# Performance work log

Measured on AMD Instinct MI355X. Metric: run time of the kernel, lower is better.

The kernel has to match this reference:

```python
import jax, jax.numpy as jnp
import numpy as np

N_QUBITS = 18
BATCH = 64
NUM_LAYERS = 4


def setup_inputs() -> dict:
    key = jax.random.key(0)
    k1, k2 = jax.random.split(key)
    inputs = jax.random.normal(k1, (BATCH, N_QUBITS), dtype=jnp.float32)
    params = jax.random.normal(k2, (NUM_LAYERS, N_QUBITS, 1), dtype=jnp.float32)
    return {"inputs": inputs, "params": params}


def _apply_shared_1q(state, U, q, B):
    # state: (B, 2^n) complex; U: (2,2) complex; qubit q (wire 0 = most significant)
    st = state.reshape(B, 2 ** q, 2, -1)
    return jnp.einsum('ij,bxjy->bxiy', U, st).reshape(B, -1)


def _apply_batched_1q(state, U, q, B):
    # U: (B,2,2) complex, per-sample gate
    st = state.reshape(B, 2 ** q, 2, -1)
    return jnp.einsum('bij,bxjy->bxiy', U, st).reshape(B, -1)


def _apply_cnot(state, q, B):
    # control = q, target = q+1: flip target amplitudes where control == 1
    st = state.reshape(B, 2 ** q, 2, 2, -1)
    flipped = jnp.flip(st[:, :, 1], axis=2)  # (B, 2^q, 2, rest)
    st = jnp.concatenate([st[:, :, :1], flipped[:, :, None]], axis=2)
    return st.reshape(B, -1)


def reference(inputs, params):
    B, n = inputs.shape
    L = params.shape[0]
    state = jnp.zeros((B, 2 ** n), dtype=jnp.complex64).at[:, 0].set(1.0)

    # data-encoding RX(inputs[:, q]) on each qubit (per-sample angles)
    half = (inputs * 0.5).astype(jnp.float32)
    c = jnp.cos(half).astype(jnp.complex64)          # (B, n)
    s = (-1j * jnp.sin(half)).astype(jnp.complex64)  # (B, n)
    for q in range(n):
        U = jnp.stack([jnp.stack([c[:, q], s[:, q]], axis=-1),
                       jnp.stack([s[:, q], c[:, q]], axis=-1)], axis=-2)  # (B,2,2)
        state = _apply_batched_1q(state, U, q, B)

    # variational blocks: RY per qubit (shared angle) + CNOT ladder
    for layer in range(L):
        for q in range(n):
            th = params[layer, q, 0] * 0.5
            cc = jnp.cos(th).astype(jnp.complex64)
            ss = jnp.sin(th).astype(jnp.complex64)
            U = jnp.stack([jnp.stack([cc, -ss]), jnp.stack([ss, cc])])  # (2,2)
            state = _apply_shared_1q(state, U, q, B)
        for q in range(n - 1):
            state = _apply_cnot(state, q, B)
    return state
```

## Files before the change

### kernel.cpp

```cpp
#include <hip/hip_runtime.h>
#include <utility>

#define NQ 18
#define BATCH 64

#define VT_OFFC (1u << 24)
#define CS_OFFC (VT_OFFC + BATCH * NQ * 4)

typedef float v2f __attribute__((ext_vector_type(2)));

__device__ __forceinline__ float2 cmulf(float2 a, float2 b) {
    return make_float2(a.x * b.x - a.y * b.y, a.x * b.y + a.y * b.x);
}

template<class F, int... Is>
__device__ __forceinline__ void unroll_impl(F f, std::integer_sequence<int, Is...>) {
    (f(std::integral_constant<int, Is>{}), ...);
}
template<int N, class F>
__device__ __forceinline__ void unroll(F f) {
    unroll_impl(f, std::make_integer_sequence<int, N>{});
}

struct Gate { int k, p; };
constexpr Gate GT[54] = {
    {2,13},{2,14},{2,15},{2,16},{2,17}, {3,14},{3,15},{3,16},{3,17}, {4,15},{4,16},{4,17},
    {2,11},{2,12}, {3,12},{3,13}, {4,13},{4,14},
    {2,8},{2,9},{2,10}, {3,9},{3,10},{3,11}, {4,10},{4,11},{4,12},
    {2,5},{2,6},{2,7}, {3,6},{3,7},{3,8}, {4,7},{4,8},{4,9},
    {2,0},{2,1},{2,2},{2,3},{2,4},
    {3,0},{3,1},{3,2},{3,3},{3,4},{3,5},
    {4,0},{4,1},{4,2},{4,3},{4,4},{4,5},{4,6},
};
constexpr unsigned gmask(Gate g) {
    return g.k == 2 ? (g.p >= 1 ? 3u << (g.p - 1) : 1u)
         : g.k == 3 ? (g.p >= 2 ? 5u << (g.p - 2) : 1u << g.p)
         : (g.p >= 3 ? 15u << (g.p - 3) : (1u << (g.p + 1)) - 1u);
}
constexpr unsigned gorient(Gate g) {
    return g.k == 2 ? (0x3FFFFu & ~((1u << g.p) - 1u))
         : g.k == 3 ? ((0x15555u << g.p) & 0x3FFFFu)
         : ((0x33333u << g.p) & 0x3FFFFu);
}
constexpr int gcsi(Gate g) { return (g.k - 2) * NQ + (17 - g.p); }

constexpr bool clsPresent(int OFF, int NG, int k, int r) {
    for (int i = 0; i < NG; ++i) {
        Gate g = GT[OFF + i];
        if (g.k == k) {
            int rr = (k == 2) ? 0 : (k == 3) ? (g.p & 1) : (g.p & 3);
            if (rr == r) return true;
        }
    }
    return false;
}

template<int WL, int OFF, int NG, int NR>
__device__ __forceinline__ void apply_gates2(v2f* A, unsigned xfix, const float* csn) {
    constexpr int NR2 = NR / 2;
    constexpr unsigned HIM = 0x3FFFFu & ~((((unsigned)NR) << WL) - 1u);

    int par2 = 0, par3[2] = {0, 0}, par4[4] = {0, 0, 0, 0};
    if constexpr (clsPresent(OFF, NG, 2, 0)) par2    = __popc(xfix & HIM) & 1;
    if constexpr (clsPresent(OFF, NG, 3, 0)) par3[0] = __popc(xfix & (HIM & 0x15555u)) & 1;
    if constexpr (clsPresent(OFF, NG, 3, 1)) par3[1] = __popc(xfix & (HIM & 0x2AAAAu)) & 1;
    if constexpr (clsPresent(OFF, NG, 4, 0)) par4[0] = __popc(xfix & (HIM & 0x33333u)) & 1;
    if constexpr (clsPresent(OFF, NG, 4, 1)) par4[1] = __popc(xfix & (HIM & 0x66666u)) & 1;
    if constexpr (clsPresent(OFF, NG, 4, 2)) par4[2] = __popc(xfix & (HIM & 0xCCCCCu)) & 1;
    if constexpr (clsPresent(OFF, NG, 4, 3)) par4[3] = __popc(xfix & (HIM & 0x99999u)) & 1;

    unroll<NG>([&](auto I) {
        constexpr Gate g = GT[OFF + I.value];
        constexpr unsigned m   = gmask(g);
        constexpr unsigned O   = gorient(g);
        constexpr unsigned mr  = (m >> WL) & (unsigned)(NR - 1);
        constexpr unsigned hb  = 1u << (g.p - WL);
        constexpr unsigned Or  = (O >> WL) & (unsigned)(NR - 1);
        constexpr unsigned Orf = Or >> 1;
        constexpr bool     Or0 = (Or & 1u) != 0;
        constexpr int clsR = (g.k == 2) ? 0 : (g.k == 3) ? (g.p & 1) : (g.p & 3);
        float c = csn[2 * gcsi(g)], s = csn[2 * gcsi(g) + 1];
        int par = (g.k == 2) ? par2 : (g.k == 3) ? par3[clsR] : par4[clsR];
        float psv = par ? -s : s;
        float msv = -psv;
        v2f cv; cv.x = c; cv.y = c;
        if constexpr ((mr & 1u) == 0u) {
            constexpr unsigned hbf = hb >> 1, mrf = mr >> 1;
            unroll<NR2>([&](auto RR) {
                constexpr int R = RR.value;
                if constexpr ((R & (int)hbf) == 0) {
                    constexpr int R2 = R ^ (int)mrf;
                    constexpr bool fl0 = (__builtin_popcount((unsigned)R & Orf) & 1) != 0;
                    constexpr bool fl1 = fl0 != Or0;
                    v2f sev; sev.x = fl0 ? msv : psv; sev.y = fl1 ? msv : psv;
                    v2f x0 = A[R], x1 = A[R2];
                    A[R]  = cv * x0 - sev * x1;
                    A[R2] = sev * x0 + cv * x1;
                }
            });
        } else if constexpr (mr == 1u) {
            unroll<NR2>([&](auto RR) {
                constexpr int R = RR.value;
                constexpr bool fl0 = (__builtin_popcount((unsigned)R & Orf) & 1) != 0;
                float se0 = fl0 ? msv : psv;
                v2f v = A[R], nv;
                nv.x = c * v.x - se0 * v.y;
                nv.y = se0 * v.x + c * v.y;
                A[R] = nv;
            });
        } else {
            constexpr unsigned hbf = hb >> 1, mrf = mr >> 1;
            unroll<NR2>([&](auto RR) {
                constexpr int R = RR.value;
                if constexpr ((R & (int)hbf) == 0) {
                    constexpr int R2 = R ^ (int)mrf;
                    constexpr bool fl0 = (__builtin_popcount((unsigned)R & Orf) & 1) != 0;
                    constexpr bool fl1 = fl0 != Or0;
                    v2f sev; sev.x = fl0 ? msv : psv; sev.y = fl1 ? msv : psv;
                    v2f x0 = A[R], x1 = A[R2];
                    v2f x1s = __builtin_shufflevector(x1, x1, 1, 0);
                    v2f t   = sev * x0;
                    v2f ts  = __builtin_shufflevector(t, t, 1, 0);
                    A[R]  = cv * x0 - sev * x1s;
                    A[R2] = ts + cv * x1;
                }
            });
        }
    });
}

template<int J>
__device__ __forceinline__ float geta(const v2f* A) {
    if constexpr (J & 1) return A[J >> 1].y; else return A[J >> 1].x;
}
template<int J>
__device__ __forceinline__ void seta(v2f* A, float v) {
    if constexpr (J & 1) A[J >> 1].y = v; else A[J >> 1].x = v;
}

__device__ __forceinline__ float4 perm4(float4 r, int k) {
    float t0 = r.x, t1 = r.y, t2 = r.z, t3 = r.w;
    if (k & 1) { float x; x=t0;t0=t1;t1=x; x=t2;t2=t3;t3=x; }
    if (k & 2) { float x; x=t0;t0=t2;t2=x; x=t1;t1=t3;t3=x; }
    return make_float4(t0, t1, t2, t3);
}

__global__ void k_prep(const float* __restrict__ inputs, const float* __restrict__ params,
                       float* __restrict__ ws) {
    int t = blockIdx.x * blockDim.x + threadIdx.x;
    if (t < BATCH * NQ) {
        int q = t % NQ;
        float x = 0.5f * inputs[t];
        float cx = cosf(x), sx = sinf(x);
        float th = 0.5f * params[q];
        float c = cosf(th), s = sinf(th);
        float* v = ws + VT_OFFC + t * 4;
        v[0] = c * cx;  v[1] = s * sx;
        v[2] = s * cx;  v[3] = -c * sx;
    } else if (t < BATCH * NQ + 54) {
        int i = t - BATCH * NQ;
        float th = 0.5f * params[NQ + i];
        ws[CS_OFFC + 2 * i]     = cosf(th);
        ws[CS_OFFC + 2 * i + 1] = sinf(th);
    }
}

__global__ __launch_bounds__(256) void k_passA(const float* __restrict__ ws_tab,
                                               float* __restrict__ ws) {
    __shared__ __align__(16) float lds[16384];
    const int b  = blockIdx.x >> 4;
    const int c4 = blockIdx.x & 15;
    const int t  = threadIdx.x;
    const float* vt  = ws_tab + VT_OFFC + b * NQ * 4;
    const float* csn = ws_tab + CS_OFFC;

    unsigned xf0 = (unsigned)c4 | ((unsigned)t << 4);
    float2 f[12];
    #pragma unroll
    for (int i = 0; i < 12; ++i) {
        int bit = (xf0 >> i) & 1;
        const float* vq = vt + (17 - i) * 4 + bit * 2;
        f[i] = make_float2(vq[0], vq[1]);
    }
    f[0] = cmulf(f[0], f[1]);  f[2] = cmulf(f[2], f[3]);
    f[4] = cmulf(f[4], f[5]);  f[6] = cmulf(f[6], f[7]);
    f[8] = cmulf(f[8], f[9]);  f[10] = cmulf(f[10], f[11]);
    f[0] = cmulf(f[0], f[2]);  f[4] = cmulf(f[4], f[6]);  f[8] = cmulf(f[8], f[10]);
    f[0] = cmulf(f[0], f[4]);
    float2 pf = cmulf(f[0], f[8]);

    float2 ca[32];
    ca[0] = pf;
    #pragma unroll
    for (int bp = 0; bp < 5; ++bp) {
        const float* vq = vt + (5 - bp) * 4;
        float2 v0 = make_float2(vq[0], vq[1]), v1 = make_float2(vq[2], vq[3]);
        #pragma unroll
        for (int i = (1 << bp) - 1; i >= 0; --i) {
            float2 base = ca[i];
            ca[i + (1 << bp)] = cmulf(base, v1);
            ca[i] = cmulf(base, v0);
        }
    }
    v2f A[32];
    {
        const float* vq = vt;
        float2 v0 = make_float2(vq[0], vq[1]), v1 = make_float2(vq[2], vq[3]);
        unroll<16>([&](auto RR) {
            constexpr int R = RR.value;
            A[R].x      = ca[2*R].x   * v0.x - ca[2*R].y   * v0.y;
            A[R].y      = ca[2*R+1].x * v0.x - ca[2*R+1].y * v0.y;
            A[16+R].x   = ca[2*R].x   * v1.x - ca[2*R].y   * v1.y;
            A[16+R].y   = ca[2*R+1].x * v1.x - ca[2*R+1].y * v1.y;
        });
    }
    apply_gates2<12, 0, 12, 64>(A, xf0, csn);

    unsigned St = (unsigned)t ^ ((unsigned)t >> 6);
    unroll<8>([&](auto Rr) {
        constexpr int r = Rr.value;
        unsigned br = St ^ (unsigned)((r << 8) | (r << 2));
        unroll<8>([&](auto Qq) {
            constexpr int q = Qq.value;
            lds[br + (q << 11)] = geta<q * 8 + r>(A);
        });
    });
    __syncthreads();

    unsigned Sb1 = (unsigned)(t & 63) | ((unsigned)(t >> 6) << 12);
    unroll<64>([&](auto J) {
        constexpr unsigned K = (unsigned)((J.value << 6) | (J.value & 31));
        seta<J.value>(A, lds[Sb1 ^ K]);
    });
    unsigned xf1 = (unsigned)c4 | ((unsigned)(t & 63) << 4) | ((unsigned)(t >> 6) << 16);
    apply_gates2<10, 12, 6, 64>(A, xf1, csn);
    unroll<64>([&](auto J) {
        constexpr unsigned K = (unsigned)((J.value << 6) | (J.value & 31));
        lds[Sb1 ^ K] = geta<J.value>(A);
    });
    __syncthreads();

    unsigned Sb2 = ((unsigned)(t & 7) | ((unsigned)(t >> 3) << 9))
                 ^ ((((unsigned)t >> 3) & 3u) << 3);
    unroll<64>([&](auto J) {
        constexpr unsigned K = (unsigned)((J.value << 3) | (J.value >> 3));
        seta<J.value>(A, lds[Sb2 ^ K]);
    });
    unsigned xf2 = (unsigned)c4 | ((unsigned)(t & 7) << 4) | ((unsigned)(t >> 3) << 13);
    apply_gates2<7, 18, 9, 64>(A, xf2, csn);
    unroll<64>([&](auto J) {
        constexpr unsigned K = (unsigned)((J.value << 3) | (J.value >> 3));
        lds[Sb2 ^ K] = geta<J.value>(A);
    });
    __syncthreads();

    unsigned Sb3 = ((unsigned)t << 6) ^ ((unsigned)t & 31u);
    unroll<64>([&](auto J) {
        seta<J.value>(A, lds[Sb3 ^ (unsigned)J.value]);
    });
    unsigned xf3 = (unsigned)c4 | ((unsigned)t << 10);
    apply_gates2<4, 27, 9, 64>(A, xf3, csn);

    float* wp = ws + (((size_t)b << 18) | ((size_t)(t >> 6) << 16)
                      | ((size_t)c4 << 9) | (size_t)(t & 63));
    unroll<64>([&](auto J) {
        constexpr int j = J.value;
        constexpr unsigned off = (unsigned)(((j >> 3) << 6) | ((j & 7) << 13));
        wp[off] = geta<j>(A);
    });
}

__global__ __launch_bounds__(256) void k_passB(const float* __restrict__ ws,
                                               float* __restrict__ out) {
    __shared__ __align__(16) float lds[8192];
    const int t = threadIdx.x;
    const int b = blockIdx.x >> 3;
    const int m = ((blockIdx.x & 7) << 8) | t;
    const float* csn = ws + CS_OFFC;
    unsigned Mv = (unsigned)m ^ ((unsigned)m >> 4);

    const float* rb = ws + (((size_t)b << 18)
                    | (size_t)((Mv >> 3) & 7u)
                    | ((size_t)((Mv >> 6) & 7u) << 3)
                    | ((size_t)(Mv & 7u) << 6)
                    | ((size_t)((Mv >> 9) & 3u) << 16));
    v2f A[64];
    unroll<128>([&](auto N) {
        constexpr int n = N.value;
        constexpr unsigned off = (unsigned)(((n & 15) << 9) | ((n >> 4) << 13));
        seta<n>(A, rb[off]);
    });
    apply_gates2<0, 36, 18, 128>(A, Mv << 7, csn);

    unsigned cc = ((unsigned)m & 15u) << 3;
    float* obb = out + (((size_t)b << NQ) | ((size_t)(blockIdx.x & 7) << 15));
    const unsigned w6 = (unsigned)(t & 63);
    const unsigned Sw = (w6 << 7) ^ ((w6 << 1) & 28u);
    const int myQ = t >> 6;
    #pragma unroll
    for (int Q = 0; Q < 4; ++Q) {
        if (myQ == Q) {
            unroll<32>([&](auto Qd) {
                constexpr int n0 = Qd.value << 2;
                unsigned nx = (unsigned)n0 ^ cc;
                unsigned D  = (nx ^ (nx >> 4)) & 127u;
                unsigned Bq = Sw ^ (D & ~3u);
                float4 v = make_float4(geta<n0>(A), geta<n0 ^ 1>(A),
                                       geta<n0 ^ 2>(A), geta<n0 ^ 3>(A));
                *(float4*)&lds[Bq] = perm4(v, (int)(D & 3u));
            });
        }
        __syncthreads();
        float* ohQ = obb + ((size_t)Q << 13);
        unroll<8>([&](auto I) {
            constexpr int i = I.value;
            unsigned p0 = ((unsigned)(i * 256) + (unsigned)t) << 2;
            unsigned z0 = p0 ^ ((p0 >> 6) & 28u);
            *(float4*)&ohQ[z0] = *(const float4*)&lds[p0];
        });
        __syncthreads();
    }
}

__global__ __launch_bounds__(256) void k_init_f(const float* __restrict__ inputs,
                                                const float* __restrict__ params,
                                                float* __restrict__ S) {
    __shared__ float2 vt[2][NQ];
    int g = blockIdx.x * 256 + threadIdx.x;
    int b = g >> 13;
    int t = threadIdx.x;
    if (t < NQ) {
        float x = 0.5f * inputs[b * NQ + t];
        float cx = cosf(x), sx = sinf(x);
        float th = 0.5f * params[t];
        float c = cosf(th), s = sinf(th);
        vt[0][t] = make_float2(c * cx,  s * sx);
        vt[1][t] = make_float2(s * cx, -c * sx);
    }
    __syncthreads();
    unsigned OW = (unsigned)(g & 0x1FFF);
    unsigned iu = OW ^ (OW >> 1);
    int pu = OW & 1;
    float2 p = make_float2(1.f, 0.f);
    #pragma unroll
    for (int q = 0; q <= 12; ++q) {
        int bit = (iu >> (12 - q)) & 1;
        p = cmulf(p, vt[bit][q]);
    }
    float2 a[32];
    a[0] = p;
    #pragma unroll
    for (int bp = 0; bp < 5; ++bp) {
        float2 v0 = vt[0][17 - bp], v1 = vt[1][17 - bp];
        if (bp == 4 && pu) { float2 tt = v0; v0 = v1; v1 = tt; }
        #pragma unroll
        for (int i = (1 << bp) - 1; i >= 0; --i) {
            float2 base = a[i];
            a[i + (1 << bp)] = cmulf(base, v1);
            a[i] = cmulf(base, v0);
        }
    }
    float* outp = S + ((size_t)b << NQ) + ((size_t)OW << 5);
    #pragma unroll
    for (int oj = 0; oj < 32; oj += 4) {
        int k0 = oj ^ (oj >> 1);
        *(float4*)(outp + oj) = make_float4(a[k0].x, a[k0 ^ 1].x, a[k0 ^ 3].x, a[k0 ^ 2].x);
    }
}

template<int P>
__global__ __launch_bounds__(256) void k_pass_f(const float* __restrict__ params,
                                                float* __restrict__ S, int layer) {
    int g = blockIdx.x * 256 + threadIdx.x;
    float cg[6], sg[6];
    #pragma unroll
    for (int i = 0; i < 6; ++i) {
        float th = 0.5f * params[layer * NQ + 6 * P + i];
        cg[i] = cosf(th); sg[i] = sinf(th);
    }
    size_t base; int hm;
    constexpr int STR = (P == 0) ? 4096 : (P == 1) ? 64 : 1;
    if constexpr (P == 0) {
        base = ((size_t)(g >> 12) << NQ) | (size_t)(g & 0xFFF);
        hm = 0;
    } else if constexpr (P == 1) {
        base = ((size_t)(g >> 12) << NQ) | ((size_t)((g >> 6) & 63) << 12) | (size_t)(g & 63);
        hm = (g >> 6) & 1;
    } else {
        base = (size_t)g << 6;
        hm = g & 1;
    }
    float a[64];
    if constexpr (P == 2) {
        #pragma unroll
        for (int j = 0; j < 64; j += 4) {
            float4 w = *(const float4*)(S + base + j);
            a[j] = w.x; a[j + 1] = w.y; a[j + 2] = w.z; a[j + 3] = w.w;
        }
    } else {
        #pragma unroll
        for (int j = 0; j < 64; ++j) a[j] = S[base + (size_t)j * STR];
    }
    #pragma unroll
    for (int i = 0; i < 6; ++i) {
        int mm = 32 >> i;
        #pragma unroll
        for (int r = 0; r < 64; ++r) if (!(r & mm)) {
            float x0 = a[r], x1 = a[r | mm];
            a[r]      = cg[i] * x0 - sg[i] * x1;
            a[r | mm] = sg[i] * x0 + cg[i] * x1;
        }
    }
    if (hm) {
        #pragma unroll
        for (int r = 0; r < 32; ++r) { float tt = a[r]; a[r] = a[r ^ 32]; a[r ^ 32] = tt; }
    }
    if constexpr (P == 2) {
        #pragma unroll
        for (int oj = 0; oj < 64; oj += 4) {
            int k0 = oj ^ (oj >> 1);
            *(float4*)(S + base + oj) = make_float4(a[k0], a[k0 ^ 1], a[k0 ^ 3], a[k0 ^ 2]);
        }
    } else {
        #pragma unroll
        for (int oj = 0; oj < 64; ++oj)
            S[base + (size_t)oj * STR] = a[oj ^ (oj >> 1)];
    }
}

extern "C" void kernel_launch(void* const* d_in, const int* in_sizes, int n_in,
                              void* d_out, int out_size, void* d_ws, size_t ws_size,
                              hipStream_t stream) {
    const float* inputs = (const float*)d_in[0];
    const float* params = (const float*)d_in[1];
    float* out = (float*)d_out;
    float* ws  = (float*)d_ws;
    const size_t need = (size_t)4 * ((1ull << 24) + BATCH * NQ * 4 + 108);

    if (ws_size >= need) {
        k_prep<<<5, 256, 0, stream>>>(inputs, params, ws);
        k_passA<<<BATCH * 16, 256, 0, stream>>>(ws, ws);
        k_passB<<<512, 256, 0, stream>>>(ws, out);
    } else {
        k_init_f<<<2048, 256, 0, stream>>>(inputs, params, out);
        for (int layer = 1; layer < 4; ++layer) {
            k_pass_f<0><<<1024, 256, 0, stream>>>(params, out, layer);
            k_pass_f<1><<<1024, 256, 0, stream>>>(params, out, layer);
            k_pass_f<2><<<1024, 256, 0, stream>>>(params, out, layer);
        }
    }
}
```

Measured before the change: 76.66 us.

## Restructure passA to 512 threads with 32 amplitudes per thread and more LDS stages

Pass A now runs 512 threads per block, each holding 32 amplitudes instead of 64, and the gate schedule is re-split into six register-local stages with five LDS transposes instead of four stages with three. The global write layout of the intermediate state changes, and pass B's read addressing is updated to match. The aim is to cut register pressure and raise occupancy and latency hiding. The cost is more shared-memory round trips and barriers per block.

```diff
diff --git a/kernel.cpp b/kernel.cpp
--- a/kernel.cpp
+++ b/kernel.cpp
@@ -24,10 +24,12 @@
 
 struct Gate { int k, p; };
 constexpr Gate GT[54] = {
-    {2,13},{2,14},{2,15},{2,16},{2,17}, {3,14},{3,15},{3,16},{3,17}, {4,15},{4,16},{4,17},
-    {2,11},{2,12}, {3,12},{3,13}, {4,13},{4,14},
-    {2,8},{2,9},{2,10}, {3,9},{3,10},{3,11}, {4,10},{4,11},{4,12},
-    {2,5},{2,6},{2,7}, {3,6},{3,7},{3,8}, {4,7},{4,8},{4,9},
+    {2,14},{2,15},{2,16},{2,17}, {3,15},{3,16},{3,17}, {4,16},{4,17},
+    {2,12},{2,13}, {3,13},{3,14}, {4,14},{4,15},
+    {2,10},{2,11}, {3,11},{3,12}, {4,12},{4,13},
+    {2,8},{2,9}, {3,9},{3,10}, {4,10},{4,11},
+    {2,6},{2,7}, {3,7},{3,8}, {4,8},{4,9},
+    {2,5}, {3,6}, {4,7},
     {2,0},{2,1},{2,2},{2,3},{2,4},
     {3,0},{3,1},{3,2},{3,3},{3,4},{3,5},
     {4,0},{4,1},{4,2},{4,3},{4,4},{4,5},{4,6},
@@ -165,7 +167,7 @@
     }
 }
 
-__global__ __launch_bounds__(256) void k_passA(const float* __restrict__ ws_tab,
+__global__ __launch_bounds__(512) void k_passA(const float* __restrict__ ws_tab,
                                                float* __restrict__ ws) {
     __shared__ __align__(16) float lds[16384];
     const int b  = blockIdx.x >> 4;
@@ -175,25 +177,24 @@
     const float* csn = ws_tab + CS_OFFC;
 
     unsigned xf0 = (unsigned)c4 | ((unsigned)t << 4);
-    float2 f[12];
-    #pragma unroll
-    for (int i = 0; i < 12; ++i) {
+    float2 f[13];
+    #pragma unroll
+    for (int i = 0; i < 13; ++i) {
         int bit = (xf0 >> i) & 1;
         const float* vq = vt + (17 - i) * 4 + bit * 2;
         f[i] = make_float2(vq[0], vq[1]);
     }
-    f[0] = cmulf(f[0], f[1]);  f[2] = cmulf(f[2], f[3]);
-    f[4] = cmulf(f[4], f[5]);  f[6] = cmulf(f[6], f[7]);
-    f[8] = cmulf(f[8], f[9]);  f[10] = cmulf(f[10], f[11]);
-    f[0] = cmulf(f[0], f[2]);  f[4] = cmulf(f[4], f[6]);  f[8] = cmulf(f[8], f[10]);
-    f[0] = cmulf(f[0], f[4]);
+    f[0]=cmulf(f[0],f[1]); f[2]=cmulf(f[2],f[3]); f[4]=cmulf(f[4],f[5]);
+    f[6]=cmulf(f[6],f[7]); f[8]=cmulf(f[8],f[9]); f[10]=cmulf(f[10],f[11]);
+    f[0]=cmulf(f[0],f[2]); f[4]=cmulf(f[4],f[6]); f[8]=cmulf(f[8],f[10]);
+    f[0]=cmulf(f[0],f[4]); f[8]=cmulf(f[8],f[12]);
     float2 pf = cmulf(f[0], f[8]);
 
-    float2 ca[32];
+    float2 ca[16];
     ca[0] = pf;
     #pragma unroll
-    for (int bp = 0; bp < 5; ++bp) {
-        const float* vq = vt + (5 - bp) * 4;
+    for (int bp = 0; bp < 4; ++bp) {
+        const float* vq = vt + (3 - bp) * 4;
         float2 v0 = make_float2(vq[0], vq[1]), v1 = make_float2(vq[2], vq[3]);
         #pragma unroll
         for (int i = (1 << bp) - 1; i >= 0; --i) {
@@ -202,71 +203,87 @@
             ca[i] = cmulf(base, v0);
         }
     }
-    v2f A[32];
+    v2f A[16];
     {
-        const float* vq = vt;
+        const float* vq = vt + 4 * 4;
         float2 v0 = make_float2(vq[0], vq[1]), v1 = make_float2(vq[2], vq[3]);
         unroll<16>([&](auto RR) {
             constexpr int R = RR.value;
-            A[R].x      = ca[2*R].x   * v0.x - ca[2*R].y   * v0.y;
-            A[R].y      = ca[2*R+1].x * v0.x - ca[2*R+1].y * v0.y;
-            A[16+R].x   = ca[2*R].x   * v1.x - ca[2*R].y   * v1.y;
-            A[16+R].y   = ca[2*R+1].x * v1.x - ca[2*R+1].y * v1.y;
+            A[R].x = ca[R].x * v0.x - ca[R].y * v0.y;
+            A[R].y = ca[R].x * v1.x - ca[R].y * v1.y;
         });
     }
-    apply_gates2<12, 0, 12, 64>(A, xf0, csn);
-
-    unsigned St = (unsigned)t ^ ((unsigned)t >> 6);
-    unroll<8>([&](auto Rr) {
-        constexpr int r = Rr.value;
-        unsigned br = St ^ (unsigned)((r << 8) | (r << 2));
-        unroll<8>([&](auto Qq) {
-            constexpr int q = Qq.value;
-            lds[br + (q << 11)] = geta<q * 8 + r>(A);
-        });
-    });
-    __syncthreads();
-
-    unsigned Sb1 = (unsigned)(t & 63) | ((unsigned)(t >> 6) << 12);
-    unroll<64>([&](auto J) {
-        constexpr unsigned K = (unsigned)((J.value << 6) | (J.value & 31));
-        seta<J.value>(A, lds[Sb1 ^ K]);
-    });
-    unsigned xf1 = (unsigned)c4 | ((unsigned)(t & 63) << 4) | ((unsigned)(t >> 6) << 16);
-    apply_gates2<10, 12, 6, 64>(A, xf1, csn);
-    unroll<64>([&](auto J) {
-        constexpr unsigned K = (unsigned)((J.value << 6) | (J.value & 31));
-        lds[Sb1 ^ K] = geta<J.value>(A);
-    });
-    __syncthreads();
-
-    unsigned Sb2 = ((unsigned)(t & 7) | ((unsigned)(t >> 3) << 9))
-                 ^ ((((unsigned)t >> 3) & 3u) << 3);
-    unroll<64>([&](auto J) {
-        constexpr unsigned K = (unsigned)((J.value << 3) | (J.value >> 3));
-        seta<J.value>(A, lds[Sb2 ^ K]);
-    });
-    unsigned xf2 = (unsigned)c4 | ((unsigned)(t & 7) << 4) | ((unsigned)(t >> 3) << 13);
-    apply_gates2<7, 18, 9, 64>(A, xf2, csn);
-    unroll<64>([&](auto J) {
-        constexpr unsigned K = (unsigned)((J.value << 3) | (J.value >> 3));
-        lds[Sb2 ^ K] = geta<J.value>(A);
-    });
-    __syncthreads();
-
-    unsigned Sb3 = ((unsigned)t << 6) ^ ((unsigned)t & 31u);
-    unroll<64>([&](auto J) {
-        seta<J.value>(A, lds[Sb3 ^ (unsigned)J.value]);
-    });
-    unsigned xf3 = (unsigned)c4 | ((unsigned)t << 10);
-    apply_gates2<4, 27, 9, 64>(A, xf3, csn);
-
-    float* wp = ws + (((size_t)b << 18) | ((size_t)(t >> 6) << 16)
-                      | ((size_t)c4 << 9) | (size_t)(t & 63));
-    unroll<64>([&](auto J) {
-        constexpr int j = J.value;
-        constexpr unsigned off = (unsigned)(((j >> 3) << 6) | ((j & 7) << 13));
-        wp[off] = geta<j>(A);
+    apply_gates2<13, 0, 9, 32>(A, xf0, csn);
+
+    unsigned S0 = (unsigned)t ^ ((unsigned)t >> 6);
+    unroll<32>([&](auto J) {
+        constexpr unsigned K = ((unsigned)J.value << 9) ^ (((unsigned)J.value & 3u) << 3);
+        lds[S0 ^ K] = geta<J.value>(A);
+    });
+    __syncthreads();
+
+    unsigned S1 = ((unsigned)(t & 127) | ((unsigned)(t >> 7) << 12)) ^ (((unsigned)t >> 6) & 1u);
+    unroll<32>([&](auto J) {
+        constexpr unsigned K = ((unsigned)J.value << 7) ^ (((unsigned)J.value & 15u) << 1);
+        seta<J.value>(A, lds[S1 ^ K]);
+    });
+    unsigned xf1 = (unsigned)c4 | ((unsigned)(t & 127) << 4) | ((unsigned)(t >> 7) << 16);
+    apply_gates2<11, 9, 6, 32>(A, xf1, csn);
+    unroll<32>([&](auto J) {
+        constexpr unsigned K = ((unsigned)J.value << 7) ^ (((unsigned)J.value & 15u) << 1);
+        lds[S1 ^ K] = geta<J.value>(A);
+    });
+    __syncthreads();
+
+    unsigned S2 = ((unsigned)(t & 31) | ((unsigned)(t >> 5) << 10)) ^ ((((unsigned)t >> 5) & 1u) << 4);
+    unroll<32>([&](auto J) {
+        constexpr unsigned K = ((unsigned)J.value << 5) ^ (((unsigned)J.value >> 1) & 15u);
+        seta<J.value>(A, lds[S2 ^ K]);
+    });
+    unsigned xf2 = (unsigned)c4 | ((unsigned)(t & 31) << 4) | ((unsigned)(t >> 5) << 14);
+    apply_gates2<9, 15, 6, 32>(A, xf2, csn);
+    unroll<32>([&](auto J) {
+        constexpr unsigned K = ((unsigned)J.value << 5) ^ (((unsigned)J.value >> 1) & 15u);
+        lds[S2 ^ K] = geta<J.value>(A);
+    });
+    __syncthreads();
+
+    unsigned S3 = ((unsigned)(t & 7) | ((unsigned)(t >> 3) << 8)) ^ ((((unsigned)t >> 3) & 7u) << 2);
+    unroll<32>([&](auto J) {
+        constexpr unsigned K = ((unsigned)J.value << 3) ^ ((unsigned)J.value >> 3);
+        seta<J.value>(A, lds[S3 ^ K]);
+    });
+    unsigned xf3 = (unsigned)c4 | ((unsigned)(t & 7) << 4) | ((unsigned)(t >> 3) << 12);
+    apply_gates2<7, 21, 6, 32>(A, xf3, csn);
+    unroll<32>([&](auto J) {
+        constexpr unsigned K = ((unsigned)J.value << 3) ^ ((unsigned)J.value >> 3);
+        lds[S3 ^ K] = geta<J.value>(A);
+    });
+    __syncthreads();
+
+    unsigned S4 = ((unsigned)(t & 1) | ((unsigned)(t >> 1) << 6)) ^ (((unsigned)t >> 1) & 31u);
+    unroll<32>([&](auto J) {
+        constexpr unsigned K = (unsigned)J.value << 1;
+        seta<J.value>(A, lds[S4 ^ K]);
+    });
+    unsigned xf4 = (unsigned)c4 | ((unsigned)(t & 1) << 4) | ((unsigned)(t >> 1) << 10);
+    apply_gates2<5, 27, 6, 32>(A, xf4, csn);
+    unroll<32>([&](auto J) {
+        constexpr unsigned K = (unsigned)J.value << 1;
+        lds[S4 ^ K] = geta<J.value>(A);
+    });
+    __syncthreads();
+
+    unsigned S5 = ((unsigned)t << 5) ^ (((unsigned)t >> 1) & 31u);
+    unroll<32>([&](auto J) {
+        seta<J.value>(A, lds[S5 ^ (unsigned)J.value]);
+    });
+    unsigned xf5 = (unsigned)c4 | ((unsigned)t << 9);
+    apply_gates2<4, 33, 3, 32>(A, xf5, csn);
+
+    float* wp = ws + (((size_t)b << 18) | ((size_t)c4 << 14) | (size_t)t);
+    unroll<32>([&](auto J) {
+        wp[(size_t)J.value << 9] = geta<J.value>(A);
     });
 }
 
@@ -280,14 +297,12 @@
     unsigned Mv = (unsigned)m ^ ((unsigned)m >> 4);
 
     const float* rb = ws + (((size_t)b << 18)
-                    | (size_t)((Mv >> 3) & 7u)
-                    | ((size_t)((Mv >> 6) & 7u) << 3)
-                    | ((size_t)(Mv & 7u) << 6)
-                    | ((size_t)((Mv >> 9) & 3u) << 16));
+                    | (size_t)((Mv >> 2) & 0x1FFu)
+                    | ((size_t)(Mv & 3u) << 12));
     v2f A[64];
     unroll<128>([&](auto N) {
         constexpr int n = N.value;
-        constexpr unsigned off = (unsigned)(((n & 15) << 9) | ((n >> 4) << 13));
+        constexpr unsigned off = (unsigned)(((n & 15) << 14) | ((n >> 4) << 9));
         seta<n>(A, rb[off]);
     });
     apply_gates2<0, 36, 18, 128>(A, Mv << 7, csn);
@@ -439,7 +454,7 @@
 
     if (ws_size >= need) {
         k_prep<<<5, 256, 0, stream>>>(inputs, params, ws);
-        k_passA<<<BATCH * 16, 256, 0, stream>>>(ws, ws);
+        k_passA<<<BATCH * 16, 512, 0, stream>>>(ws, ws);
         k_passB<<<512, 256, 0, stream>>>(ws, out);
     } else {
         k_init_f<<<2048, 256, 0, stream>>>(inputs, params, out);
```

Measured after the change: 85.95 us. 12.1% more time.
